# Performance work log

Hardware: AMD Instinct MI355X
Metric: run time of the kernel (lower is better)

The kernel has to match this reference:

```python
import jax, jax.numpy as jnp
import numpy as np

BN_EPS = 1e-5


def _gin_layer(x, src, dst, n_nodes, W1, b1, W2, b2, gamma, beta):
    # GINConv with eps=0: z_i = x_i + sum_{(j->i) in E} x_j, then 2-layer MLP
    agg = jax.ops.segment_sum(x[src], dst, num_segments=n_nodes)  # [N, d]
    z = x + agg
    z = jax.nn.relu(z @ W1 + b1) @ W2 + b2
    # BatchNorm1d (training mode: biased batch statistics over node dim)
    mean = jnp.mean(z, axis=0)
    var = jnp.var(z, axis=0)
    z = (z - mean) * jax.lax.rsqrt(var + BN_EPS) * gamma + beta
    return jax.nn.relu(z)  # dropout p=0 -> identity


def setup_inputs() -> dict:
    key = jax.random.key(0)
    ks = jax.random.split(key, 8)
    N, E, D, L = 50000, 800000, 128, 2
    h = jax.random.normal(ks[0], (N, D), dtype=jnp.float32)
    edge_index = jax.random.randint(ks[1], (2, E), 0, N, dtype=jnp.int64)
    scale = 1.0 / np.sqrt(D)
    W1 = jax.random.normal(ks[2], (L, D, D), dtype=jnp.float32) * scale
    b1 = jax.random.normal(ks[3], (L, D), dtype=jnp.float32) * 0.01
    W2 = jax.random.normal(ks[4], (L, D, D), dtype=jnp.float32) * scale
    b2 = jax.random.normal(ks[5], (L, D), dtype=jnp.float32) * 0.01
    gamma = jnp.ones((L, D), dtype=jnp.float32)
    beta = jnp.zeros((L, D), dtype=jnp.float32)
    return {"h": h, "edge_index": edge_index, "W1": W1, "b1": b1,
            "W2": W2, "b2": b2, "gamma": gamma, "beta": beta}


def reference(h, edge_index, W1, b1, W2, b2, gamma, beta):
    src, dst = edge_index[0], edge_index[1]
    n_nodes = h.shape[0]
    n_layers = W1.shape[0]
    outs = []
    x = h
    for i in range(n_layers):
        x = _gin_layer(x, src, dst, n_nodes, W1[i], b1[i], W2[i], b2[i], gamma[i], beta[i])
        outs.append(x)
    return jnp.stack(outs)  # [L, N, D] == hs[1:]
```

## Files before the change

kernel.cpp:

```cpp
#include <hip/hip_runtime.h>

#define D 128
#define BN_EPS 1e-5f

typedef __attribute__((ext_vector_type(8))) short short8;
typedef __attribute__((ext_vector_type(4))) float f32x4;

__device__ inline unsigned short f2bf(float f) {
    union { float f; unsigned int u; } v; v.f = f;
    unsigned int u = v.u;
    unsigned int r = (u + 0x7FFFu + ((u >> 16) & 1u)) >> 16;
    return (unsigned short)r;
}

__device__ inline float bfbits2f(unsigned int bits) {
    union { unsigned int u; float f; } v; v.u = bits;
    return v.f;
}

__device__ inline float4 bf2f4(uint2 v) {
    float4 r;
    r.x = bfbits2f(v.x << 16);
    r.y = bfbits2f(v.x & 0xFFFF0000u);
    r.z = bfbits2f(v.y << 16);
    r.w = bfbits2f(v.y & 0xFFFF0000u);
    return r;
}

__global__ void prep_all(const float* __restrict__ W1, const float* __restrict__ W2,
                         unsigned short* __restrict__ Wt,
                         const float* __restrict__ h, unsigned short* __restrict__ xb,
                         int* __restrict__ cnt, float* __restrict__ stats,
                         int* __restrict__ done, int N, int L, int n8) {
    const int nth = gridDim.x * blockDim.x;
    const int tid = blockIdx.x * blockDim.x + threadIdx.x;
    if (tid == 0) *done = 0;
    for (int i = tid; i < N; i += nth) cnt[i] = 0;
    for (int i = tid; i < 2 * D * L; i += nth) stats[i] = 0.f;
    const int nw = 2 * L * D * D;
    for (int idx = tid; idx < nw; idx += nth) {
        int m = idx >> 14;
        int rem = idx & 16383;
        int c = rem >> 7, k = rem & 127;
        const float* W = (m < L) ? (W1 + (size_t)m * D * D) : (W2 + (size_t)(m - L) * D * D);
        Wt[(size_t)m * D * D + c * D + k] = f2bf(W[k * D + c]);
    }
    for (int i = tid; i < n8; i += nth) {
        float4 a = reinterpret_cast<const float4*>(h)[2 * i];
        float4 b = reinterpret_cast<const float4*>(h)[2 * i + 1];
        uint4 o;
        o.x = (unsigned)f2bf(a.x) | ((unsigned)f2bf(a.y) << 16);
        o.y = (unsigned)f2bf(a.z) | ((unsigned)f2bf(a.w) << 16);
        o.z = (unsigned)f2bf(b.x) | ((unsigned)f2bf(b.y) << 16);
        o.w = (unsigned)f2bf(b.z) | ((unsigned)f2bf(b.w) << 16);
        reinterpret_cast<uint4*>(xb)[i] = o;
    }
}

__global__ void hist_rank(const int* __restrict__ dst, int* __restrict__ cnt,
                          int* __restrict__ rank, int E) {
    int e = blockIdx.x * blockDim.x + threadIdx.x;
    if (e >= E) return;
    rank[e] = atomicAdd(&cnt[dst[e]], 1);
}

__global__ void reduce_scan(const int* __restrict__ cnt, int* __restrict__ bsum,
                            int* __restrict__ blockOff, int* __restrict__ offN,
                            int* __restrict__ done, int n, int nb) {
    __shared__ int s[256];
    __shared__ int isLast;
    int tid = threadIdx.x;
    int i = blockIdx.x * 256 + tid;
    s[tid] = (i < n) ? cnt[i] : 0;
    __syncthreads();
    for (int ofs = 128; ofs > 0; ofs >>= 1) {
        if (tid < ofs) s[tid] += s[tid + ofs];
        __syncthreads();
    }
    if (tid == 0) {
        bsum[blockIdx.x] = s[0];
        __threadfence();
        isLast = (atomicAdd(done, 1) == nb - 1) ? 1 : 0;
    }
    __syncthreads();
    if (isLast) {
        __threadfence();
        int v = (tid < nb) ? bsum[tid] : 0;
        s[tid] = v;
        __syncthreads();
        for (int ofs = 1; ofs < 256; ofs <<= 1) {
            int t2 = (tid >= ofs) ? s[tid - ofs] : 0;
            __syncthreads();
            s[tid] += t2;
            __syncthreads();
        }
        if (tid < nb) blockOff[tid] = s[tid] - v;
        if (tid == nb - 1) *offN = s[tid];
    }
}

__global__ void scan_partial(const int* __restrict__ cnt, int* __restrict__ off,
                             const int* __restrict__ blockOff, int n) {
    __shared__ int s[256];
    int tid = threadIdx.x;
    int i = blockIdx.x * 256 + tid;
    int v = (i < n) ? cnt[i] : 0;
    s[tid] = v;
    __syncthreads();
    for (int ofs = 1; ofs < 256; ofs <<= 1) {
        int t = (tid >= ofs) ? s[tid - ofs] : 0;
        __syncthreads();
        s[tid] += t;
        __syncthreads();
    }
    if (i < n) off[i] = blockOff[blockIdx.x] + s[tid] - v;
}

template<typename IdxT>
__global__ void fill2(const int* __restrict__ src, const int* __restrict__ dst,
                      const int* __restrict__ rank, const int* __restrict__ off,
                      IdxT* __restrict__ eidx, int E) {
    int e = blockIdx.x * blockDim.x + threadIdx.x;
    if (e >= E) return;
    __builtin_nontemporal_store((IdxT)src[e], &eidx[off[dst[e]] + rank[e]]);
}

template<typename IdxT>
__global__ __launch_bounds__(256) void gather_bf(
        const unsigned short* __restrict__ xb, const int* __restrict__ off,
        const IdxT* __restrict__ eidx, unsigned short* __restrict__ zb, int N) {
    int t = blockIdx.x * blockDim.x + threadIdx.x;
    int node = t >> 5;
    if (node >= N) return;
    int lane = t & 31;
    int beg = off[node], end = off[node + 1];
    float4 acc = bf2f4(*reinterpret_cast<const uint2*>(xb + (size_t)node * D + lane * 4));
    int e = beg;
    for (; e + 2 <= end; e += 2) {
        int s0 = (int)eidx[e], s1 = (int)eidx[e + 1];
        uint2 v0 = *reinterpret_cast<const uint2*>(xb + (size_t)s0 * D + lane * 4);
        uint2 v1 = *reinterpret_cast<const uint2*>(xb + (size_t)s1 * D + lane * 4);
        float4 f0 = bf2f4(v0), f1 = bf2f4(v1);
        acc.x += f0.x + f1.x; acc.y += f0.y + f1.y;
        acc.z += f0.z + f1.z; acc.w += f0.w + f1.w;
    }
    if (e < end) {
        int s0 = (int)eidx[e];
        float4 f0 = bf2f4(*reinterpret_cast<const uint2*>(xb + (size_t)s0 * D + lane * 4));
        acc.x += f0.x; acc.y += f0.y; acc.z += f0.z; acc.w += f0.w;
    }
    unsigned long long packed =
        ((unsigned long long)((unsigned)f2bf(acc.z) | ((unsigned)f2bf(acc.w) << 16)) << 32) |
        (unsigned long long)((unsigned)f2bf(acc.x) | ((unsigned)f2bf(acc.y) << 16));
    __builtin_nontemporal_store(packed,
        reinterpret_cast<unsigned long long*>(zb + (size_t)node * D + lane * 4));
}

__global__ __launch_bounds__(256) void gemm1_mfma(
        const unsigned short* __restrict__ A, const unsigned short* __restrict__ Wt,
        const float* __restrict__ bias, unsigned short* __restrict__ Out, int N) {
    const int tid = threadIdx.x;
    const int lane = tid & 63, wv = tid >> 6;
    const int r0 = blockIdx.x * 128 + wv * 32;
    const int koff = (lane >> 4) << 3;
    const int col = lane & 15;

    int ar0 = r0 + col;       if (ar0 >= N) ar0 = N - 1;
    int ar1 = r0 + 16 + col;  if (ar1 >= N) ar1 = N - 1;
    const unsigned short* ap0 = A + (size_t)ar0 * D + koff;
    const unsigned short* ap1 = A + (size_t)ar1 * D + koff;
    const unsigned short* wp  = Wt + (size_t)col * D + koff;

    f32x4 acc[2][8];
    #pragma unroll
    for (int ct = 0; ct < 8; ct++) {
        float b = bias[ct * 16 + col];
        acc[0][ct] = (f32x4){b, b, b, b};
        acc[1][ct] = (f32x4){b, b, b, b};
    }
    #pragma unroll
    for (int ks = 0; ks < 4; ks++) {
        short8 a0 = *reinterpret_cast<const short8*>(ap0 + ks * 32);
        short8 a1 = *reinterpret_cast<const short8*>(ap1 + ks * 32);
        #pragma unroll
        for (int ct = 0; ct < 8; ct++) {
            short8 bfr = *reinterpret_cast<const short8*>(wp + (size_t)ct * 16 * D + ks * 32);
            acc[0][ct] = __builtin_amdgcn_mfma_f32_16x16x32_bf16(a0, bfr, acc[0][ct], 0, 0, 0);
            acc[1][ct] = __builtin_amdgcn_mfma_f32_16x16x32_bf16(a1, bfr, acc[1][ct], 0, 0, 0);
        }
    }
    #pragma unroll
    for (int t = 0; t < 2; t++) {
        #pragma unroll
        for (int ct = 0; ct < 8; ct++) {
            #pragma unroll
            for (int r = 0; r < 4; r++) {
                int row = r0 + t * 16 + ((lane >> 4) << 2) + r;
                if (row < N)
                    Out[(size_t)row * D + ct * 16 + col] = f2bf(fmaxf(acc[t][ct][r], 0.f));
            }
        }
    }
}

__global__ __launch_bounds__(256) void gemm2_mfma(
        const unsigned short* __restrict__ A, const unsigned short* __restrict__ Wt,
        const float* __restrict__ bias, float* __restrict__ Out,
        float* __restrict__ gstats, int N) {
    __shared__ float sStat[2 * D];
    const int tid = threadIdx.x;
    if (tid < 2 * D) sStat[tid] = 0.f;
    __syncthreads();

    const int lane = tid & 63, wv = tid >> 6;
    const int r0 = blockIdx.x * 128 + wv * 32;
    const int koff = (lane >> 4) << 3;
    const int col = lane & 15;

    int ar0 = r0 + col;       if (ar0 >= N) ar0 = N - 1;
    int ar1 = r0 + 16 + col;  if (ar1 >= N) ar1 = N - 1;
    const unsigned short* ap0 = A + (size_t)ar0 * D + koff;
    const unsigned short* ap1 = A + (size_t)ar1 * D + koff;
    const unsigned short* wp  = Wt + (size_t)col * D + koff;

    f32x4 acc[2][8];
    #pragma unroll
    for (int ct = 0; ct < 8; ct++) {
        float b = bias[ct * 16 + col];
        acc[0][ct] = (f32x4){b, b, b, b};
        acc[1][ct] = (f32x4){b, b, b, b};
    }
    #pragma unroll
    for (int ks = 0; ks < 4; ks++) {
        short8 a0 = *reinterpret_cast<const short8*>(ap0 + ks * 32);
        short8 a1 = *reinterpret_cast<const short8*>(ap1 + ks * 32);
        #pragma unroll
        for (int ct = 0; ct < 8; ct++) {
            short8 bfr = *reinterpret_cast<const short8*>(wp + (size_t)ct * 16 * D + ks * 32);
            acc[0][ct] = __builtin_amdgcn_mfma_f32_16x16x32_bf16(a0, bfr, acc[0][ct], 0, 0, 0);
            acc[1][ct] = __builtin_amdgcn_mfma_f32_16x16x32_bf16(a1, bfr, acc[1][ct], 0, 0, 0);
        }
    }
    #pragma unroll
    for (int ct = 0; ct < 8; ct++) {
        float s = 0.f, q = 0.f;
        #pragma unroll
        for (int t = 0; t < 2; t++) {
            #pragma unroll
            for (int r = 0; r < 4; r++) {
                int row = r0 + t * 16 + ((lane >> 4) << 2) + r;
                float v = acc[t][ct][r];
                if (row < N) {
                    Out[(size_t)row * D + ct * 16 + col] = v;
                    s += v; q += v * v;
                }
            }
        }
        s += __shfl_xor(s, 16); q += __shfl_xor(q, 16);
        s += __shfl_xor(s, 32); q += __shfl_xor(q, 32);
        if (lane < 16) {
            atomicAdd(&sStat[ct * 16 + lane], s);
            atomicAdd(&sStat[D + ct * 16 + lane], q);
        }
    }
    __syncthreads();
    if (tid < 2 * D) atomicAdd(&gstats[tid], sStat[tid]);
}

__global__ void bn_relu_bf(float* __restrict__ y, unsigned short* __restrict__ xb,
                           const float* __restrict__ stats,
                           const float* __restrict__ gamma, const float* __restrict__ beta,
                           int N, int emit_bf) {
    int i = blockIdx.x * blockDim.x + threadIdx.x;
    int n4 = N * D / 4;
    if (i >= n4) return;
    int c0 = (i << 2) & (D - 1);
    float4 v = reinterpret_cast<float4*>(y)[i];
    float o[4] = {v.x, v.y, v.z, v.w};
    float invN = 1.0f / (float)N;
    #pragma unroll
    for (int j = 0; j < 4; j++) {
        int c = c0 + j;
        float mean = stats[c] * invN;
        float var  = stats[D + c] * invN - mean * mean;
        float sc = rsqrtf(var + BN_EPS) * gamma[c];
        float t = (o[j] - mean) * sc + beta[c];
        o[j] = fmaxf(t, 0.f);
    }
    float4 r; r.x = o[0]; r.y = o[1]; r.z = o[2]; r.w = o[3];
    reinterpret_cast<float4*>(y)[i] = r;
    if (emit_bf) {
        uint2 ob;
        ob.x = (unsigned)f2bf(o[0]) | ((unsigned)f2bf(o[1]) << 16);
        ob.y = (unsigned)f2bf(o[2]) | ((unsigned)f2bf(o[3]) << 16);
        reinterpret_cast<uint2*>(xb)[i] = ob;
    }
}

extern "C" void kernel_launch(void* const* d_in, const int* in_sizes, int n_in,
                              void* d_out, int out_size, void* d_ws, size_t ws_size,
                              hipStream_t stream) {
    const float* h     = (const float*)d_in[0];
    const int*   ei    = (const int*)d_in[1];
    const float* W1    = (const float*)d_in[2];
    const float* b1    = (const float*)d_in[3];
    const float* W2    = (const float*)d_in[4];
    const float* b2    = (const float*)d_in[5];
    const float* gamma = (const float*)d_in[6];
    const float* beta  = (const float*)d_in[7];
    float* out = (float*)d_out;

    const int N = in_sizes[0] / D;
    const int E = in_sizes[1] / 2;
    const int L = in_sizes[2] / (D * D);
    const int nb = (N + 255) / 256;

    unsigned short* zb  = (unsigned short*)d_ws;
    unsigned short* xb  = zb + (size_t)N * D;
    unsigned short* Wt  = xb + (size_t)N * D;
    float* stats = (float*)(Wt + (size_t)2 * L * D * D);
    int* cnt      = (int*)(stats + (size_t)L * 2 * D);
    int* off      = cnt + N;
    int* bsum     = off + N + 1;
    int* blockOff = bsum + nb;
    int* done     = blockOff + nb;
    int* rank     = done + 1;
    void* eidx    = (void*)(rank + E);

    const int* src = ei;
    const int* dst = ei + E;

    const int n4 = N * D / 4;
    const int n8 = N * D / 8;
    const int ewBlocks = (E + 255) / 256;
    const int gatherBlocks = (N * 32 + 255) / 256;
    const int gemmBlocks = (N + 127) / 128;
    const int bnBlocks = (n4 + 255) / 256;
    const bool small = (N <= 65535);

    prep_all<<<1024, 256, 0, stream>>>(W1, W2, Wt, h, xb, cnt, stats, done, N, L, n8);

    hist_rank<<<ewBlocks, 256, 0, stream>>>(dst, cnt, rank, E);
    reduce_scan<<<nb, 256, 0, stream>>>(cnt, bsum, blockOff, off + N, done, N, nb);
    scan_partial<<<nb, 256, 0, stream>>>(cnt, off, blockOff, N);
    if (small)
        fill2<unsigned short><<<ewBlocks, 256, 0, stream>>>(src, dst, rank, off,
                                                            (unsigned short*)eidx, E);
    else
        fill2<int><<<ewBlocks, 256, 0, stream>>>(src, dst, rank, off, (int*)eidx, E);

    for (int l = 0; l < L; l++) {
        float* y = out + (size_t)l * N * D;
        const unsigned short* Wt1 = Wt + (size_t)l * D * D;
        const unsigned short* Wt2 = Wt + (size_t)(L + l) * D * D;

        if (small)
            gather_bf<unsigned short><<<gatherBlocks, 256, 0, stream>>>(
                xb, off, (const unsigned short*)eidx, zb, N);
        else
            gather_bf<int><<<gatherBlocks, 256, 0, stream>>>(
                xb, off, (const int*)eidx, zb, N);

        gemm1_mfma<<<gemmBlocks, 256, 0, stream>>>(zb, Wt1, b1 + (size_t)l * D, zb, N);
        gemm2_mfma<<<gemmBlocks, 256, 0, stream>>>(zb, Wt2, b2 + (size_t)l * D,
                                                   y, stats + (size_t)l * 2 * D, N);
        bn_relu_bf<<<bnBlocks, 256, 0, stream>>>(y, xb, stats + (size_t)l * 2 * D,
                                                 gamma + (size_t)l * D, beta + (size_t)l * D,
                                                 N, (l + 1 < L) ? 1 : 0);
    }
}
```

Before: 249.2 us.

## Partition gather feature columns by XCD with atomic work queues for L2 locality

The gather kernel is restructured so each block reads its XCC ID and takes work from a per-slice atomic queue. Each of four slices owns 32 of the 128 feature columns, so a given XCD's L2 only caches a quarter of the bf16 feature matrix. Blocks whose slice queue is empty steal from the other slices. The aim is to raise L2 hit rates on the random neighbour gathers. In exchange it adds per-block atomics, 4x more blocks, narrower 8-lane-per-node loads with lower memory coalescing, and it relies on the XCC ID hardware register (MI355X has 8 XCDs, but only 4 slices are used).

```diff
diff --git a/kernel.cpp b/kernel.cpp
--- a/kernel.cpp
+++ b/kernel.cpp
@@ -31,10 +31,12 @@
                          unsigned short* __restrict__ Wt,
                          const float* __restrict__ h, unsigned short* __restrict__ xb,
                          int* __restrict__ cnt, float* __restrict__ stats,
-                         int* __restrict__ done, int N, int L, int n8) {
+                         int* __restrict__ done, int* __restrict__ qcnt,
+                         int N, int L, int n8) {
     const int nth = gridDim.x * blockDim.x;
     const int tid = blockIdx.x * blockDim.x + threadIdx.x;
     if (tid == 0) *done = 0;
+    if (tid < 8) qcnt[tid] = 0;
     for (int i = tid; i < N; i += nth) cnt[i] = 0;
     for (int i = tid; i < 2 * D * L; i += nth) stats[i] = 0.f;
     const int nw = 2 * L * D * D;
@@ -126,34 +128,56 @@
 }
 
 template<typename IdxT>
-__global__ __launch_bounds__(256) void gather_bf(
+__global__ __launch_bounds__(256) void gather_bf_xcd(
         const unsigned short* __restrict__ xb, const int* __restrict__ off,
-        const IdxT* __restrict__ eidx, unsigned short* __restrict__ zb, int N) {
-    int t = blockIdx.x * blockDim.x + threadIdx.x;
-    int node = t >> 5;
+        const IdxT* __restrict__ eidx, unsigned short* __restrict__ zb,
+        int* __restrict__ qcnt, int N, int nodeBlocks) {
+    __shared__ int sWork, sSlice;
+    if (threadIdx.x == 0) {
+        unsigned xcc = 0;
+        asm volatile("s_getreg_b32 %0, hwreg(HW_REG_XCC_ID)" : "=s"(xcc));
+        int sl = (int)(xcc & 3u);
+        int idx = atomicAdd(&qcnt[sl], 1);
+        if (idx >= nodeBlocks) {
+            idx = -1;
+            #pragma unroll
+            for (int k = 1; k <= 3; k++) {
+                int t = (sl + k) & 3;
+                int j = atomicAdd(&qcnt[t], 1);
+                if (j < nodeBlocks) { sl = t; idx = j; break; }
+            }
+        }
+        sWork = idx; sSlice = sl;
+    }
+    __syncthreads();
+    const int widx = sWork;
+    if (widx < 0) return;
+    const int node = widx * 32 + (threadIdx.x >> 3);
     if (node >= N) return;
-    int lane = t & 31;
+    const int lane8 = threadIdx.x & 7;
+    const int colOfs = sSlice * 32 + lane8 * 4;
+    const unsigned short* base = xb + colOfs;
+
+    float4 acc = bf2f4(*reinterpret_cast<const uint2*>(base + (size_t)node * D));
     int beg = off[node], end = off[node + 1];
-    float4 acc = bf2f4(*reinterpret_cast<const uint2*>(xb + (size_t)node * D + lane * 4));
     int e = beg;
     for (; e + 2 <= end; e += 2) {
         int s0 = (int)eidx[e], s1 = (int)eidx[e + 1];
-        uint2 v0 = *reinterpret_cast<const uint2*>(xb + (size_t)s0 * D + lane * 4);
-        uint2 v1 = *reinterpret_cast<const uint2*>(xb + (size_t)s1 * D + lane * 4);
+        uint2 v0 = *reinterpret_cast<const uint2*>(base + (size_t)s0 * D);
+        uint2 v1 = *reinterpret_cast<const uint2*>(base + (size_t)s1 * D);
         float4 f0 = bf2f4(v0), f1 = bf2f4(v1);
         acc.x += f0.x + f1.x; acc.y += f0.y + f1.y;
         acc.z += f0.z + f1.z; acc.w += f0.w + f1.w;
     }
     if (e < end) {
         int s0 = (int)eidx[e];
-        float4 f0 = bf2f4(*reinterpret_cast<const uint2*>(xb + (size_t)s0 * D + lane * 4));
+        float4 f0 = bf2f4(*reinterpret_cast<const uint2*>(base + (size_t)s0 * D));
         acc.x += f0.x; acc.y += f0.y; acc.z += f0.z; acc.w += f0.w;
     }
-    unsigned long long packed =
-        ((unsigned long long)((unsigned)f2bf(acc.z) | ((unsigned)f2bf(acc.w) << 16)) << 32) |
-        (unsigned long long)((unsigned)f2bf(acc.x) | ((unsigned)f2bf(acc.y) << 16));
-    __builtin_nontemporal_store(packed,
-        reinterpret_cast<unsigned long long*>(zb + (size_t)node * D + lane * 4));
+    uint2 o;
+    o.x = (unsigned)f2bf(acc.x) | ((unsigned)f2bf(acc.y) << 16);
+    o.y = (unsigned)f2bf(acc.z) | ((unsigned)f2bf(acc.w) << 16);
+    *reinterpret_cast<uint2*>(zb + (size_t)node * D + colOfs) = o;
 }
 
 __global__ __launch_bounds__(256) void gemm1_mfma(
@@ -324,7 +348,8 @@
     int* bsum     = off + N + 1;
     int* blockOff = bsum + nb;
     int* done     = blockOff + nb;
-    int* rank     = done + 1;
+    int* qcnt     = done + 1;
+    int* rank     = qcnt + 8;
     void* eidx    = (void*)(rank + E);
 
     const int* src = ei;
@@ -333,12 +358,13 @@
     const int n4 = N * D / 4;
     const int n8 = N * D / 8;
     const int ewBlocks = (E + 255) / 256;
-    const int gatherBlocks = (N * 32 + 255) / 256;
+    const int nodeBlocks = (N + 31) / 32;
+    const int gatherBlocks = 4 * nodeBlocks;
     const int gemmBlocks = (N + 127) / 128;
     const int bnBlocks = (n4 + 255) / 256;
     const bool small = (N <= 65535);
 
-    prep_all<<<1024, 256, 0, stream>>>(W1, W2, Wt, h, xb, cnt, stats, done, N, L, n8);
+    prep_all<<<1024, 256, 0, stream>>>(W1, W2, Wt, h, xb, cnt, stats, done, qcnt, N, L, n8);
 
     hist_rank<<<ewBlocks, 256, 0, stream>>>(dst, cnt, rank, E);
     reduce_scan<<<nb, 256, 0, stream>>>(cnt, bsum, blockOff, off + N, done, N, nb);
@@ -355,11 +381,11 @@
         const unsigned short* Wt2 = Wt + (size_t)(L + l) * D * D;
 
         if (small)
-            gather_bf<unsigned short><<<gatherBlocks, 256, 0, stream>>>(
-                xb, off, (const unsigned short*)eidx, zb, N);
+            gather_bf_xcd<unsigned short><<<gatherBlocks, 256, 0, stream>>>(
+                xb, off, (const unsigned short*)eidx, zb, qcnt + 4 * l, N, nodeBlocks);
         else
-            gather_bf<int><<<gatherBlocks, 256, 0, stream>>>(
-                xb, off, (const int*)eidx, zb, N);
+            gather_bf_xcd<int><<<gatherBlocks, 256, 0, stream>>>(
+                xb, off, (const int*)eidx, zb, qcnt + 4 * l, N, nodeBlocks);
 
         gemm1_mfma<<<gemmBlocks, 256, 0, stream>>>(zb, Wt1, b1 + (size_t)l * D, zb, N);
         gemm2_mfma<<<gemmBlocks, 256, 0, stream>>>(zb, Wt2, b2 + (size_t)l * D,
```

After: 340.2 us. +36.5%, slower.
